# Kernel tuning notes

Measured on AMD Instinct MI355X. Metric: run time of the kernel, lower is better.

Reference implementation:

```python
import jax, jax.numpy as jnp
import numpy as np

B, S, H = 2, 2048, 1024
NH, NKV, HD = 16, 16, 64
R, KF = 16, 4
THETA = 1000000.0


def setup_inputs() -> dict:
    key = jax.random.key(0)
    ks = jax.random.split(key, 16)
    sc = 0.02
    signs = jax.random.randint(ks[13], (1, 1, 1, KF, HD // 2), 0, 2).astype(jnp.float32) * 2 - 1
    cdma = jnp.concatenate([signs, signs], axis=-1)  # [1,1,1,KF,HD]
    return {
        "hidden_states": jax.random.normal(ks[0], (B, S, H), jnp.float32),
        "position_ids": jnp.broadcast_to(jnp.arange(S, dtype=jnp.int32), (B, S)),
        "q_w": jax.random.normal(ks[1], (H, H), jnp.float32) * sc,
        "q_b": jax.random.normal(ks[2], (H,), jnp.float32) * sc,
        "k_w": jax.random.normal(ks[3], (H, H), jnp.float32) * sc,
        "k_b": jax.random.normal(ks[4], (H,), jnp.float32) * sc,
        "v_w": jax.random.normal(ks[5], (H, H), jnp.float32) * sc,
        "v_b": jax.random.normal(ks[6], (H,), jnp.float32) * sc,
        "o_w": jax.random.normal(ks[7], (H, H), jnp.float32) * sc,
        "lora_qA": jax.random.normal(ks[8], (R, H), jnp.float32) * sc,
        "lora_qB": jax.random.normal(ks[9], (H, R), jnp.float32) * sc,
        "lora_vA": jax.random.normal(ks[10], (R, H), jnp.float32) * sc,
        "lora_vB": jax.random.normal(ks[11], (H, R), jnp.float32) * sc,
        "cdma_keys": cdma,
    }


def _rope(q, k, position_ids):
    # cos/sin per HF rotary embedding, theta=1e6 (Qwen1.5)
    inv_freq = 1.0 / (THETA ** (jnp.arange(0, HD, 2, dtype=jnp.float32) / HD))  # [HD/2]
    freqs = position_ids.astype(jnp.float32)[..., None] * inv_freq  # [B,S,HD/2]
    emb = jnp.concatenate([freqs, freqs], axis=-1)  # [B,S,HD]
    cos = jnp.cos(emb)[:, None]  # [B,1,S,HD]
    sin = jnp.sin(emb)[:, None]

    def rot_half(x):
        return jnp.concatenate([-x[..., HD // 2:], x[..., :HD // 2]], axis=-1)

    return q * cos + rot_half(q) * sin, k * cos + rot_half(k) * sin


def reference(hidden_states, position_ids, q_w, q_b, k_w, k_b, v_w, v_b, o_w,
              lora_qA, lora_qB, lora_vA, lora_vB, cdma_keys):
    bsz, q_len, _ = hidden_states.shape
    # base projections + LoRA adjustments (k has no LoRA)
    q = hidden_states @ q_w.T + q_b + (hidden_states @ lora_qA.T) @ lora_qB.T
    k = hidden_states @ k_w.T + k_b
    v = hidden_states @ v_w.T + v_b + (hidden_states @ lora_vA.T) @ lora_vB.T

    q = q.reshape(bsz, q_len, NH, HD).transpose(0, 2, 1, 3)   # [B,NH,S,HD]
    k = k.reshape(bsz, q_len, NKV, HD).transpose(0, 2, 1, 3)  # [B,NKV,S,HD]
    v = v.reshape(bsz, q_len, NKV, HD).transpose(0, 2, 1, 3)

    q, k = _rope(q, k, position_ids)

    # holographic block sign-bind/sum transform (q_len divisible by KF -> no pad)
    n_slots = q_len // KF
    k_blocks = k.reshape(bsz, NKV, n_slots, KF, HD)
    v_blocks = v.reshape(bsz, NKV, n_slots, KF, HD)
    S_K = jnp.sum(k_blocks * cdma_keys, axis=3, keepdims=True)  # [B,NKV,slots,1,HD]
    S_V = jnp.sum(v_blocks * cdma_keys, axis=3, keepdims=True)
    K_noisy = (S_K * cdma_keys).reshape(bsz, NKV, q_len, HD)
    V_noisy = (S_V * cdma_keys).reshape(bsz, NKV, q_len, HD)

    scale = 1.0 / (np.sqrt(HD) * np.sqrt(KF))
    scores = jnp.einsum('bhqd,bhkd->bhqk', q, K_noisy) * scale
    causal = jnp.tril(jnp.ones((q_len, q_len), dtype=bool))
    scores = jnp.where(causal, scores, jnp.float32(-1e9))
    attn = jax.nn.softmax(scores, axis=-1)
    out = jnp.einsum('bhqk,bhkd->bhqd', attn, V_noisy)
    out = out.transpose(0, 2, 1, 3).reshape(bsz, q_len, NH * HD)
    return out @ o_w.T
```

## Files before the change

### kernel.cpp

```cpp
#include <hip/hip_runtime.h>
#include <hip/hip_bf16.h>
#include <math.h>


typedef __bf16 bf16;
typedef __attribute__((ext_vector_type(8))) __bf16 bf16x8;
typedef __attribute__((ext_vector_type(4))) float f32x4;
typedef __attribute__((ext_vector_type(2))) unsigned u32x2;

#define NB 2
#define SEQ 2048
#define HID 1024
#define NHD 16
#define HDD 64

__device__ __forceinline__ void gld_lds16(const void* g, void* l) {
  __builtin_amdgcn_global_load_lds(
      (const __attribute__((address_space(1))) void*)g,
      (__attribute__((address_space(3))) void*)l, 16, 0, 0);
}

__device__ __forceinline__ unsigned pack2bf(float a, float b) {
  unsigned short ua = __builtin_bit_cast(unsigned short, (bf16)a);
  unsigned short ub = __builtin_bit_cast(unsigned short, (bf16)b);
  return ((unsigned)ub << 16) | ua;
}

#define RB_W    12288
#define RB_HS   (RB_W + 16384)
#define RB_OW   (RB_HS + 4096)
#define RB_BIAS (RB_OW + 12)
#define RB_TAB  (RB_BIAS + 256)

__global__ __launch_bounds__(256) void prep_all(
    const float* __restrict__ hs, const float* __restrict__ ow,
    const float* __restrict__ qw, const float* __restrict__ qb,
    const float* __restrict__ kw, const float* __restrict__ kb,
    const float* __restrict__ vw, const float* __restrict__ vb,
    const float* __restrict__ qA, const float* __restrict__ qB,
    const float* __restrict__ vA, const float* __restrict__ vB,
    bf16* __restrict__ hsb, bf16* __restrict__ owb, bf16* __restrict__ Wqkv,
    float* __restrict__ bqkv, float* __restrict__ ct, float* __restrict__ st) {
  const int bid = blockIdx.x, tid = threadIdx.x;
  if (bid < RB_W) {
    int idx = bid * 256 + tid;
    int n = idx >> 10, k = idx & 1023;
    float v;
    if (n < 1024) {
      v = qw[n * 1024 + k];
#pragma unroll
      for (int r = 0; r < 16; ++r) v += qB[n * 16 + r] * qA[r * 1024 + k];
    } else if (n < 2048) {
      v = kw[(n - 1024) * 1024 + k];
    } else {
      int nn = n - 2048;
      v = vw[nn * 1024 + k];
#pragma unroll
      for (int r = 0; r < 16; ++r) v += vB[nn * 16 + r] * vA[r * 1024 + k];
    }
    int seg = k >> 6, cl = k & 63;
    int ch = (cl >> 3) ^ (n & 7);
    Wqkv[(size_t)n * 1024 + (seg << 6) + (ch << 3) + (cl & 7)] = (bf16)v;
  } else if (bid < RB_HS) {
    int idx = (bid - RB_W) * 256 + tid;
    int r = idx >> 10, c = idx & 1023;
    int seg = c >> 6, cl = c & 63;
    int ch = (cl >> 3) ^ (r & 7);
    hsb[(size_t)r * 1024 + (seg << 6) + (ch << 3) + (cl & 7)] = (bf16)hs[idx];
  } else if (bid < RB_OW) {
    int idx = (bid - RB_HS) * 256 + tid;
    int r = idx >> 10, c = idx & 1023;
    int seg = c >> 6, cl = c & 63;
    int ch = (cl >> 3) ^ (r & 7);
    owb[(size_t)r * 1024 + (seg << 6) + (ch << 3) + (cl & 7)] = (bf16)ow[idx];
  } else if (bid < RB_BIAS) {
    int i = (bid - RB_OW) * 256 + tid;
    if (i < 3072)
      bqkv[i] = (i < 1024) ? qb[i] : (i < 2048 ? kb[i - 1024] : vb[i - 2048]);
  } else {
    int idx = (bid - RB_BIAS) * 256 + tid;
    int s = idx >> 5, i = idx & 31;
    double inv = pow(1.0e6, -(double)i / 32.0);
    double a = (double)s * inv;
    ct[idx] = (float)cos(a);
    st[idx] = (float)sin(a);
  }
}

__global__ __launch_bounds__(256) void gemm_bt(
    const bf16* __restrict__ A, const bf16* __restrict__ Bw,
    const float* __restrict__ bias, bf16* __restrict__ Cb,
    float* __restrict__ Cf, int M, int N, int K) {
  __shared__ __align__(16) bf16 As[128 * 64];
  __shared__ __align__(16) bf16 Bs[128 * 64];
  const int tid = threadIdx.x;
  const int lane = tid & 63, w = tid >> 6;
  const int wm = w >> 1, wn = w & 1;
  const int l15 = lane & 15, l4 = lane >> 4;
  const int m0 = blockIdx.y * 128, n0 = blockIdx.x * 128;
  const size_t rowb = (size_t)K * 2;
  const char* gA = (const char*)A + (size_t)m0 * rowb;
  const char* gB = (const char*)Bw + (size_t)n0 * rowb;
  f32x4 acc[4][4] = {};

  for (int k0 = 0; k0 < K; k0 += 64) {
    const char* gAk = gA + k0 * 2;
    const char* gBk = gB + k0 * 2;
#pragma unroll
    for (int i = 0; i < 4; ++i) {
      int idx = i * 256 + tid;
      int row = idx >> 3, ch = idx & 7;
      gld_lds16(gAk + (size_t)row * rowb + ch * 16,
                (char*)As + (i * 256 + (w << 6)) * 16);
      gld_lds16(gBk + (size_t)row * rowb + ch * 16,
                (char*)Bs + (i * 256 + (w << 6)) * 16);
    }
    __syncthreads();
#pragma unroll
    for (int c = 0; c < 2; ++c) {
      bf16x8 af[4], bfr[4];
#pragma unroll
      for (int mi = 0; mi < 4; ++mi) {
        int row = wm * 64 + mi * 16 + l15;
        int ch = (c * 4 + l4) ^ (row & 7);
        af[mi] = *(const bf16x8*)(As + row * 64 + ch * 8);
      }
#pragma unroll
      for (int ni = 0; ni < 4; ++ni) {
        int row = wn * 64 + ni * 16 + l15;
        int ch = (c * 4 + l4) ^ (row & 7);
        bfr[ni] = *(const bf16x8*)(Bs + row * 64 + ch * 8);
      }
#pragma unroll
      for (int mi = 0; mi < 4; ++mi)
#pragma unroll
        for (int ni = 0; ni < 4; ++ni)
          acc[mi][ni] = __builtin_amdgcn_mfma_f32_16x16x32_bf16(
              af[mi], bfr[ni], acc[mi][ni], 0, 0, 0);
    }
    __syncthreads();
  }
#pragma unroll
  for (int mi = 0; mi < 4; ++mi) {
    int rbase = m0 + wm * 64 + mi * 16 + l4 * 4;
#pragma unroll
    for (int ni = 0; ni < 4; ++ni) {
      int col = n0 + wn * 64 + ni * 16 + l15;
      float badd = bias ? bias[col] : 0.0f;
#pragma unroll
      for (int r = 0; r < 4; ++r) {
        float v = acc[mi][ni][r] + badd;
        if (Cf) Cf[(size_t)(rbase + r) * N + col] = v;
        else    Cb[(size_t)(rbase + r) * N + col] = (bf16)v;
      }
    }
  }
}

__global__ __launch_bounds__(256) void rope_q(
    const bf16* __restrict__ qkv, const int* __restrict__ pos,
    const float* __restrict__ ct, const float* __restrict__ st,
    bf16* __restrict__ Qr) {
  const float SCQ = 0.0901684403f;
  int idx = blockIdx.x * 256 + threadIdx.x;
  if (idx >= NB * NHD * SEQ * 4) return;
  int ih = idx & 3, s = (idx >> 2) & 2047, h = (idx >> 13) & 15, b = idx >> 17;
  int p = pos[b * SEQ + s];
  size_t base = ((size_t)(b * SEQ + s)) * 3072 + h * 64 + ih * 8;
  bf16x8 xv = *(const bf16x8*)(qkv + base);
  bf16x8 yv = *(const bf16x8*)(qkv + base + 32);
  const float* ctp = ct + p * 32 + ih * 8;
  const float* stp = st + p * 32 + ih * 8;
  bf16x8 o0, o1;
#pragma unroll
  for (int e = 0; e < 8; ++e) {
    float x = (float)xv[e], y = (float)yv[e];
    float co = ctp[e], sn = stp[e];
    o0[e] = (bf16)((x * co - y * sn) * SCQ);
    o1[e] = (bf16)((y * co + x * sn) * SCQ);
  }
  size_t ob = ((size_t)((b * 16 + h) * SEQ + s)) * 64 + ih * 8;
  *(bf16x8*)(Qr + ob) = o0;
  *(bf16x8*)(Qr + ob + 32) = o1;
}

__global__ __launch_bounds__(256) void holo_kv(
    const bf16* __restrict__ qkv, const int* __restrict__ pos,
    const float* __restrict__ ct, const float* __restrict__ st,
    const float* __restrict__ cdma, bf16* __restrict__ Kn,
    bf16* __restrict__ Vt) {
  int idx = blockIdx.x * 256 + threadIdx.x;
  if (idx >= NB * NHD * (SEQ / 4) * 4) return;
  int ih = idx & 3, slot = (idx >> 2) & 511, h = (idx >> 11) & 15, b = idx >> 15;
  float SK[8] = {}, SK2[8] = {}, SV[8] = {}, SV2[8] = {};
#pragma unroll
  for (int f = 0; f < 4; ++f) {
    int s = slot * 4 + f;
    size_t base = ((size_t)(b * SEQ + s)) * 3072 + h * 64 + ih * 8;
    bf16x8 klo = *(const bf16x8*)(qkv + base + 1024);
    bf16x8 khi = *(const bf16x8*)(qkv + base + 1024 + 32);
    bf16x8 vlo = *(const bf16x8*)(qkv + base + 2048);
    bf16x8 vhi = *(const bf16x8*)(qkv + base + 2048 + 32);
    int p = pos[b * SEQ + s];
    const float* ctp = ct + p * 32 + ih * 8;
    const float* stp = st + p * 32 + ih * 8;
    const float* cdp = cdma + f * 64 + ih * 8;
#pragma unroll
    for (int e = 0; e < 8; ++e) {
      float cf = cdp[e];
      float kx = (float)klo[e], ky = (float)khi[e];
      float co = ctp[e], sn = stp[e];
      SK[e]  += (kx * co - ky * sn) * cf;
      SK2[e] += (ky * co + kx * sn) * cf;
      SV[e]  += (float)vlo[e] * cf;
      SV2[e] += (float)vhi[e] * cf;
    }
  }
  size_t hb = (size_t)(b * 16 + h);
#pragma unroll
  for (int f = 0; f < 4; ++f) {
    int s = slot * 4 + f;
    const float* cdp = cdma + f * 64 + ih * 8;
    bf16x8 k0, k1;
#pragma unroll
    for (int e = 0; e < 8; ++e) {
      k0[e] = (bf16)(SK[e] * cdp[e]);
      k1[e] = (bf16)(SK2[e] * cdp[e]);
    }
    size_t krow = (hb * SEQ + s) * 64;
    int ch0 = ih ^ (s & 7);
    int ch1 = (4 + ih) ^ (s & 7);
    *(bf16x8*)(Kn + krow + ch0 * 8) = k0;
    *(bf16x8*)(Kn + krow + ch1 * 8) = k1;
    int seg = s >> 6, cl = s & 63;
    size_t vcol = (size_t)(seg << 6) + (cl & 7);
#pragma unroll
    for (int e = 0; e < 8; ++e) {
      int i = ih * 8 + e;
      int vch = (cl >> 3) ^ (i & 7);
      Vt[(hb * 64 + i) * (size_t)SEQ + vcol + vch * 8] = (bf16)(SV[e] * cdp[e]);
      Vt[(hb * 64 + i + 32) * (size_t)SEQ + vcol + vch * 8] = (bf16)(SV2[e] * cdp[e]);
    }
  }
}

__global__ __launch_bounds__(256) void attn_fwd(
    const bf16* __restrict__ Qr, const bf16* __restrict__ Kn,
    const bf16* __restrict__ Vt, bf16* __restrict__ AO) {
  __shared__ __align__(16) bf16 Kt[2][128 * 64];
  __shared__ __align__(16) bf16 Vl[2][64 * 128];
  __shared__ __align__(16) bf16 Pt[4][16 * 128];
  const int pq = blockIdx.x, h = blockIdx.y, b = blockIdx.z;
  const int tid = threadIdx.x, lane = tid & 63, w = tid >> 6;
  const int l15 = lane & 15, l4 = lane >> 4;
  const size_t hd = ((size_t)(b * 16 + h)) * SEQ * 64;
  const char* gK0 = (const char*)(Kn + hd);
  const char* gV0 = (const char*)(Vt + hd);
  char* pw = (char*)&Pt[w][0];

#pragma unroll 1
  for (int phase = 0; phase < 2; ++phase) {
    const int qt = phase ? (31 - pq) : pq;
    const int q0 = qt * 64;
    const int qg = q0 + w * 16 + l15;
    const int nt = (qt >> 1) + 1;

    const bf16* qb = Qr + hd + (size_t)qg * 64;
    bf16x8 qf0 = *(const bf16x8*)(qb + l4 * 8);
    bf16x8 qf1 = *(const bf16x8*)(qb + 32 + l4 * 8);

    f32x4 oacc[4] = {};
    float m = -1e30f, lsum = 0.0f;

#pragma unroll
    for (int i = 0; i < 4; ++i)
      gld_lds16(gK0 + (i * 256 + tid) * 16,
                (char*)Kt[0] + (i * 256 + (w << 6)) * 16);
#pragma unroll
    for (int i = 0; i < 4; ++i) {
      int idx = i * 256 + tid;
      int row = idx >> 4, ch = idx & 15;
      gld_lds16(gV0 + (size_t)row * (SEQ * 2) + ch * 16,
                (char*)Vl[0] + (i * 256 + (w << 6)) * 16);
    }

#pragma unroll 1
    for (int t = 0; t < nt; ++t) {
      const int cur = t & 1;
      if (t + 1 < nt) {
        const int tn = t + 1, sb = cur ^ 1;
#pragma unroll
        for (int i = 0; i < 4; ++i)
          gld_lds16(gK0 + (size_t)tn * 16384 + (i * 256 + tid) * 16,
                    (char*)Kt[sb] + (i * 256 + (w << 6)) * 16);
#pragma unroll
        for (int i = 0; i < 4; ++i) {
          int idx = i * 256 + tid;
          int row = idx >> 4, ch = idx & 15;
          gld_lds16(gV0 + (size_t)row * (SEQ * 2) + tn * 256 + ch * 16,
                    (char*)Vl[sb] + (i * 256 + (w << 6)) * 16);
        }
        asm volatile("s_waitcnt vmcnt(8)\ns_barrier" ::: "memory");
      } else {
        asm volatile("s_waitcnt vmcnt(0)\ns_barrier" ::: "memory");
      }

      const bf16* Ktc = Kt[cur];
      const bf16* Vlc = Vl[cur];
      const int kv0 = t * 128;
      const bool lastt = (t == nt - 1);

      f32x4 sacc[8] = {};
#pragma unroll
      for (int c = 0; c < 2; ++c) {
        bf16x8 qf = c ? qf1 : qf0;
#pragma unroll
        for (int nf = 0; nf < 8; ++nf) {
          int row = nf * 16 + l15;
          int ch = (c * 4 + l4) ^ (row & 7);
          bf16x8 kf = *(const bf16x8*)(Ktc + row * 64 + ch * 8);
          sacc[nf] = __builtin_amdgcn_mfma_f32_16x16x32_bf16(kf, qf, sacc[nf], 0, 0, 0);
        }
      }

      float px[4] = {-1e30f, -1e30f, -1e30f, -1e30f};
      if (lastt) {
#pragma unroll
        for (int nf = 0; nf < 8; ++nf)
#pragma unroll
          for (int r = 0; r < 4; ++r) {
            int kvg = kv0 + nf * 16 + l4 * 4 + r;
            float v = (kvg > qg) ? -1e30f : sacc[nf][r];
            sacc[nf][r] = v;
            px[nf & 3] = fmaxf(px[nf & 3], v);
          }
      } else {
#pragma unroll
        for (int nf = 0; nf < 8; ++nf)
#pragma unroll
          for (int r = 0; r < 4; ++r) px[nf & 3] = fmaxf(px[nf & 3], sacc[nf][r]);
      }
      float pmax = fmaxf(fmaxf(px[0], px[1]), fmaxf(px[2], px[3]));
      pmax = fmaxf(pmax, __shfl_xor(pmax, 16));
      pmax = fmaxf(pmax, __shfl_xor(pmax, 32));

      if (!__all(pmax <= m)) {
        float mn = fmaxf(m, pmax);
        float al = exp2f(m - mn);
        m = mn;
        lsum *= al;
#pragma unroll
        for (int df = 0; df < 4; ++df) oacc[df] *= al;
      }
      float rs4[4] = {0.f, 0.f, 0.f, 0.f};
#pragma unroll
      for (int nf = 0; nf < 8; ++nf)
#pragma unroll
        for (int r = 0; r < 4; ++r) {
          float e = exp2f(sacc[nf][r] - m);
          sacc[nf][r] = e;
          rs4[nf & 3] += e;
        }
      float rs = (rs4[0] + rs4[1]) + (rs4[2] + rs4[3]);
      rs += __shfl_xor(rs, 16);
      rs += __shfl_xor(rs, 32);
      lsum += rs;

#pragma unroll
      for (int nf = 0; nf < 8; ++nf) {
        u32x2 u;
        u.x = pack2bf(sacc[nf][0], sacc[nf][1]);
        u.y = pack2bf(sacc[nf][2], sacc[nf][3]);
        int boff = (l15 * 256 + nf * 32 + l4 * 8) ^ ((l15 & 7) << 4);
        *(u32x2*)(pw + boff) = u;
      }

#pragma unroll
      for (int c2 = 0; c2 < 4; ++c2) {
        int pb = (l15 * 256 + c2 * 64 + l4 * 16) ^ ((l15 & 7) << 4);
        bf16x8 pf = *(const bf16x8*)(pw + pb);
        int vbyte = (c2 * 64 + l4 * 16) ^ ((l15 & 7) << 4);
#pragma unroll
        for (int df = 0; df < 4; ++df) {
          int vrow = df * 16 + l15;
          bf16x8 vf = *(const bf16x8*)((const char*)Vlc + vrow * 256 + vbyte);
          oacc[df] = __builtin_amdgcn_mfma_f32_16x16x32_bf16(vf, pf, oacc[df], 0, 0, 0);
        }
      }
      asm volatile("s_barrier" ::: "memory");
    }

    const float li = 1.0f / lsum;
    const size_t arow = ((size_t)(b * SEQ + qg)) * HID + h * 64;
    const int qk7 = qg & 7;
#pragma unroll
    for (int df = 0; df < 4; ++df)
#pragma unroll
      for (int r = 0; r < 4; ++r) {
        int d = df * 16 + l4 * 4 + r;
        int ch = (d >> 3) ^ qk7;
        AO[arow + ch * 8 + (d & 7)] = (bf16)(oacc[df][r] * li);
      }
  }
}

extern "C" void kernel_launch(void* const* d_in, const int* in_sizes, int n_in,
                              void* d_out, int out_size, void* d_ws, size_t ws_size,
                              hipStream_t stream) {
  const float* hs  = (const float*)d_in[0];
  const int* pos   = (const int*)d_in[1];
  const float* qw  = (const float*)d_in[2];
  const float* qb_ = (const float*)d_in[3];
  const float* kw  = (const float*)d_in[4];
  const float* kb_ = (const float*)d_in[5];
  const float* vw  = (const float*)d_in[6];
  const float* vb_ = (const float*)d_in[7];
  const float* ow  = (const float*)d_in[8];
  const float* qA  = (const float*)d_in[9];
  const float* qB  = (const float*)d_in[10];
  const float* vA  = (const float*)d_in[11];
  const float* vB  = (const float*)d_in[12];
  const float* cd  = (const float*)d_in[13];

  char* p = (char*)d_ws;
  auto alloc = [&](size_t bytes) {
    char* r = p; p += (bytes + 255) & ~(size_t)255; return r;
  };
  bf16* hsb   = (bf16*)alloc((size_t)4096 * 1024 * 2);
  bf16* Wqkv  = (bf16*)alloc((size_t)3072 * 1024 * 2);
  float* bqkv = (float*)alloc(3072 * 4);
  bf16* owb   = (bf16*)alloc((size_t)1024 * 1024 * 2);
  bf16* qkvb  = (bf16*)alloc((size_t)4096 * 3072 * 2);
  float* ct   = (float*)alloc((size_t)SEQ * 32 * 4);
  float* st   = (float*)alloc((size_t)SEQ * 32 * 4);
  bf16* Qrb   = (bf16*)alloc((size_t)NB * NHD * SEQ * 64 * 2);
  bf16* Knb   = (bf16*)alloc((size_t)NB * NHD * SEQ * 64 * 2);
  bf16* Vtb   = (bf16*)alloc((size_t)NB * NHD * 64 * SEQ * 2);
  bf16* AOb   = (bf16*)alloc((size_t)4096 * 1024 * 2);

  prep_all<<<dim3(RB_TAB), 256, 0, stream>>>(
      hs, ow, qw, qb_, kw, kb_, vw, vb_, qA, qB, vA, vB,
      hsb, owb, Wqkv, bqkv, ct, st);
  gemm_bt<<<dim3(3072 / 128, 4096 / 128), 256, 0, stream>>>(
      hsb, Wqkv, bqkv, qkvb, nullptr, 4096, 3072, 1024);
  rope_q<<<dim3(NB * NHD * SEQ * 4 / 256), 256, 0, stream>>>(qkvb, pos, ct, st, Qrb);
  holo_kv<<<dim3(NB * NHD * (SEQ / 4) * 4 / 256), 256, 0, stream>>>(
      qkvb, pos, ct, st, cd, Knb, Vtb);
  attn_fwd<<<dim3(16, NHD, NB), 256, 0, stream>>>(Qrb, Knb, Vtb, AOb);
  gemm_bt<<<dim3(1024 / 128, 4096 / 128), 256, 0, stream>>>(
      AOb, owb, nullptr, nullptr, (float*)d_out, 4096, 1024, 1024);
}
```

Baseline: 158.2 us.

## Fuse RoPE and holographic K/V transform into QKV GEMM epilogue

Replaces the QKV GEMM, the separate rope_q kernel and the holo_kv kernel with one GEMM whose epilogue applies bias, RoPE, the Q scale, and the block sign-bind/sum on K and V. It writes Qr, Kn and the transposed Vt directly, so the intermediate bf16 qkv buffer is no longer written and read back and two launches go away. In exchange the epilogue does scattered scalar bf16 stores and per-element table lookups, which may be less coalesced than the old vectorised kernels.

```diff
diff --git a/kernel.cpp b/kernel.cpp
--- a/kernel.cpp
+++ b/kernel.cpp
@@ -87,9 +87,149 @@
   }
 }
 
+__global__ __launch_bounds__(256) void gemm_qkv(
+    const bf16* __restrict__ A, const bf16* __restrict__ Bw,
+    const float* __restrict__ bias, const int* __restrict__ pos,
+    const float* __restrict__ ct, const float* __restrict__ st,
+    const float* __restrict__ cd, bf16* __restrict__ Qr,
+    bf16* __restrict__ Kn, bf16* __restrict__ Vt) {
+  __shared__ __align__(16) bf16 As[128 * 64];
+  __shared__ __align__(16) bf16 Bs[128 * 64];
+  const int tid = threadIdx.x;
+  const int lane = tid & 63, w = tid >> 6;
+  const int wm = w >> 1, wn = w & 1;
+  const int l15 = lane & 15, l4 = lane >> 4;
+  const int m0 = blockIdx.y * 128, n0 = blockIdx.x * 128;
+  const int K = 1024;
+  const size_t rowb = (size_t)K * 2;
+  const char* gA = (const char*)A + (size_t)m0 * rowb;
+  const char* gB = (const char*)Bw + (size_t)n0 * rowb;
+  f32x4 acc[4][4] = {};
+
+  for (int k0 = 0; k0 < K; k0 += 64) {
+    const char* gAk = gA + k0 * 2;
+    const char* gBk = gB + k0 * 2;
+#pragma unroll
+    for (int i = 0; i < 4; ++i) {
+      int idx = i * 256 + tid;
+      int row = idx >> 3, ch = idx & 7;
+      gld_lds16(gAk + (size_t)row * rowb + ch * 16,
+                (char*)As + (i * 256 + (w << 6)) * 16);
+      gld_lds16(gBk + (size_t)row * rowb + ch * 16,
+                (char*)Bs + (i * 256 + (w << 6)) * 16);
+    }
+    __syncthreads();
+#pragma unroll
+    for (int c = 0; c < 2; ++c) {
+      bf16x8 af[4], bfr[4];
+#pragma unroll
+      for (int mi = 0; mi < 4; ++mi) {
+        int row = wm * 64 + mi * 16 + l15;
+        int ch = (c * 4 + l4) ^ (row & 7);
+        af[mi] = *(const bf16x8*)(As + row * 64 + ch * 8);
+      }
+#pragma unroll
+      for (int ni = 0; ni < 4; ++ni) {
+        int row = wn * 64 + ni * 16 + l15;
+        int ch = (c * 4 + l4) ^ (row & 7);
+        bfr[ni] = *(const bf16x8*)(Bs + row * 64 + ch * 8);
+      }
+#pragma unroll
+      for (int mi = 0; mi < 4; ++mi)
+#pragma unroll
+        for (int ni = 0; ni < 4; ++ni)
+          acc[mi][ni] = __builtin_amdgcn_mfma_f32_16x16x32_bf16(
+              af[mi], bfr[ni], acc[mi][ni], 0, 0, 0);
+    }
+    __syncthreads();
+  }
+
+  const float SCQ = 0.0901684403f;
+  const int nb0 = n0 + wn * 64;
+  const int region = nb0 >> 10;
+  const int h = (nb0 & 1023) >> 6;
+
+#pragma unroll
+  for (int mi = 0; mi < 4; ++mi) {
+    const int sg0 = m0 + wm * 64 + mi * 16 + l4 * 4;
+    const int b = sg0 >> 11, s0 = sg0 & 2047;
+    const size_t hb = (size_t)(b * 16 + h);
+    if (region == 0) {
+#pragma unroll
+      for (int ni = 0; ni < 2; ++ni) {
+        const int i = ni * 16 + l15;
+        const float bx = bias[nb0 + i];
+        const float by = bias[nb0 + i + 32];
+#pragma unroll
+        for (int r = 0; r < 4; ++r) {
+          int s = s0 + r;
+          int p = pos[sg0 + r];
+          float co = ct[p * 32 + i], sn = st[p * 32 + i];
+          float x = acc[mi][ni][r] + bx;
+          float y = acc[mi][ni + 2][r] + by;
+          size_t ob = (hb * SEQ + s) * 64 + i;
+          Qr[ob]      = (bf16)((x * co - y * sn) * SCQ);
+          Qr[ob + 32] = (bf16)((y * co + x * sn) * SCQ);
+        }
+      }
+    } else if (region == 1) {
+#pragma unroll
+      for (int ni = 0; ni < 2; ++ni) {
+        const int i = ni * 16 + l15;
+        const float bx = bias[nb0 + i];
+        const float by = bias[nb0 + i + 32];
+        float cdv[4];
+        float SK = 0.f, SK2 = 0.f, rot0[4], rot1[4];
+#pragma unroll
+        for (int r = 0; r < 4; ++r) {
+          int p = pos[sg0 + r];
+          float co = ct[p * 32 + i], sn = st[p * 32 + i];
+          float x = acc[mi][ni][r] + bx;
+          float y = acc[mi][ni + 2][r] + by;
+          rot0[r] = x * co - y * sn;
+          rot1[r] = y * co + x * sn;
+          float cf = cd[r * 64 + i];
+          cdv[r] = cf;
+          SK  += rot0[r] * cf;
+          SK2 += rot1[r] * cf;
+        }
+#pragma unroll
+        for (int r = 0; r < 4; ++r) {
+          int s = s0 + r;
+          size_t krow = (hb * SEQ + s) * 64;
+          int ch0 = (i >> 3) ^ (s & 7);
+          int ch1 = (4 + (i >> 3)) ^ (s & 7);
+          Kn[krow + ch0 * 8 + (i & 7)] = (bf16)(SK * cdv[r]);
+          Kn[krow + ch1 * 8 + (i & 7)] = (bf16)(SK2 * cdv[r]);
+        }
+      }
+    } else {
+#pragma unroll
+      for (int ni = 0; ni < 4; ++ni) {
+        const int i = ni * 16 + l15;
+        const float bv = bias[nb0 + i];
+        float cdv[4];
+        float SV = 0.f;
+#pragma unroll
+        for (int r = 0; r < 4; ++r) {
+          float cf = cd[r * 64 + i];
+          cdv[r] = cf;
+          SV += (acc[mi][ni][r] + bv) * cf;
+        }
+        int seg = s0 >> 6, cl = s0 & 63;
+        int vch = (cl >> 3) ^ (i & 7);
+        size_t voff = (hb * 64 + i) * (size_t)SEQ + (seg << 6) + vch * 8 + (cl & 7);
+        u32x2 u;
+        u.x = pack2bf(SV * cdv[0], SV * cdv[1]);
+        u.y = pack2bf(SV * cdv[2], SV * cdv[3]);
+        *(u32x2*)(Vt + voff) = u;
+      }
+    }
+  }
+}
+
 __global__ __launch_bounds__(256) void gemm_bt(
     const bf16* __restrict__ A, const bf16* __restrict__ Bw,
-    const float* __restrict__ bias, bf16* __restrict__ Cb,
     float* __restrict__ Cf, int M, int N, int K) {
   __shared__ __align__(16) bf16 As[128 * 64];
   __shared__ __align__(16) bf16 Bs[128 * 64];
@@ -146,100 +286,9 @@
 #pragma unroll
     for (int ni = 0; ni < 4; ++ni) {
       int col = n0 + wn * 64 + ni * 16 + l15;
-      float badd = bias ? bias[col] : 0.0f;
-#pragma unroll
-      for (int r = 0; r < 4; ++r) {
-        float v = acc[mi][ni][r] + badd;
-        if (Cf) Cf[(size_t)(rbase + r) * N + col] = v;
-        else    Cb[(size_t)(rbase + r) * N + col] = (bf16)v;
-      }
-    }
-  }
-}
-
-__global__ __launch_bounds__(256) void rope_q(
-    const bf16* __restrict__ qkv, const int* __restrict__ pos,
-    const float* __restrict__ ct, const float* __restrict__ st,
-    bf16* __restrict__ Qr) {
-  const float SCQ = 0.0901684403f;
-  int idx = blockIdx.x * 256 + threadIdx.x;
-  if (idx >= NB * NHD * SEQ * 4) return;
-  int ih = idx & 3, s = (idx >> 2) & 2047, h = (idx >> 13) & 15, b = idx >> 17;
-  int p = pos[b * SEQ + s];
-  size_t base = ((size_t)(b * SEQ + s)) * 3072 + h * 64 + ih * 8;
-  bf16x8 xv = *(const bf16x8*)(qkv + base);
-  bf16x8 yv = *(const bf16x8*)(qkv + base + 32);
-  const float* ctp = ct + p * 32 + ih * 8;
-  const float* stp = st + p * 32 + ih * 8;
-  bf16x8 o0, o1;
-#pragma unroll
-  for (int e = 0; e < 8; ++e) {
-    float x = (float)xv[e], y = (float)yv[e];
-    float co = ctp[e], sn = stp[e];
-    o0[e] = (bf16)((x * co - y * sn) * SCQ);
-    o1[e] = (bf16)((y * co + x * sn) * SCQ);
-  }
-  size_t ob = ((size_t)((b * 16 + h) * SEQ + s)) * 64 + ih * 8;
-  *(bf16x8*)(Qr + ob) = o0;
-  *(bf16x8*)(Qr + ob + 32) = o1;
-}
-
-__global__ __launch_bounds__(256) void holo_kv(
-    const bf16* __restrict__ qkv, const int* __restrict__ pos,
-    const float* __restrict__ ct, const float* __restrict__ st,
-    const float* __restrict__ cdma, bf16* __restrict__ Kn,
-    bf16* __restrict__ Vt) {
-  int idx = blockIdx.x * 256 + threadIdx.x;
-  if (idx >= NB * NHD * (SEQ / 4) * 4) return;
-  int ih = idx & 3, slot = (idx >> 2) & 511, h = (idx >> 11) & 15, b = idx >> 15;
-  float SK[8] = {}, SK2[8] = {}, SV[8] = {}, SV2[8] = {};
-#pragma unroll
-  for (int f = 0; f < 4; ++f) {
-    int s = slot * 4 + f;
-    size_t base = ((size_t)(b * SEQ + s)) * 3072 + h * 64 + ih * 8;
-    bf16x8 klo = *(const bf16x8*)(qkv + base + 1024);
-    bf16x8 khi = *(const bf16x8*)(qkv + base + 1024 + 32);
-    bf16x8 vlo = *(const bf16x8*)(qkv + base + 2048);
-    bf16x8 vhi = *(const bf16x8*)(qkv + base + 2048 + 32);
-    int p = pos[b * SEQ + s];
-    const float* ctp = ct + p * 32 + ih * 8;
-    const float* stp = st + p * 32 + ih * 8;
-    const float* cdp = cdma + f * 64 + ih * 8;
-#pragma unroll
-    for (int e = 0; e < 8; ++e) {
-      float cf = cdp[e];
-      float kx = (float)klo[e], ky = (float)khi[e];
-      float co = ctp[e], sn = stp[e];
-      SK[e]  += (kx * co - ky * sn) * cf;
-      SK2[e] += (ky * co + kx * sn) * cf;
-      SV[e]  += (float)vlo[e] * cf;
-      SV2[e] += (float)vhi[e] * cf;
-    }
-  }
-  size_t hb = (size_t)(b * 16 + h);
-#pragma unroll
-  for (int f = 0; f < 4; ++f) {
-    int s = slot * 4 + f;
-    const float* cdp = cdma + f * 64 + ih * 8;
-    bf16x8 k0, k1;
-#pragma unroll
-    for (int e = 0; e < 8; ++e) {
-      k0[e] = (bf16)(SK[e] * cdp[e]);
-      k1[e] = (bf16)(SK2[e] * cdp[e]);
-    }
-    size_t krow = (hb * SEQ + s) * 64;
-    int ch0 = ih ^ (s & 7);
-    int ch1 = (4 + ih) ^ (s & 7);
-    *(bf16x8*)(Kn + krow + ch0 * 8) = k0;
-    *(bf16x8*)(Kn + krow + ch1 * 8) = k1;
-    int seg = s >> 6, cl = s & 63;
-    size_t vcol = (size_t)(seg << 6) + (cl & 7);
-#pragma unroll
-    for (int e = 0; e < 8; ++e) {
-      int i = ih * 8 + e;
-      int vch = (cl >> 3) ^ (i & 7);
-      Vt[(hb * 64 + i) * (size_t)SEQ + vcol + vch * 8] = (bf16)(SV[e] * cdp[e]);
-      Vt[(hb * 64 + i + 32) * (size_t)SEQ + vcol + vch * 8] = (bf16)(SV2[e] * cdp[e]);
+#pragma unroll
+      for (int r = 0; r < 4; ++r)
+        Cf[(size_t)(rbase + r) * N + col] = acc[mi][ni][r];
     }
   }
 }
@@ -430,7 +479,6 @@
   bf16* Wqkv  = (bf16*)alloc((size_t)3072 * 1024 * 2);
   float* bqkv = (float*)alloc(3072 * 4);
   bf16* owb   = (bf16*)alloc((size_t)1024 * 1024 * 2);
-  bf16* qkvb  = (bf16*)alloc((size_t)4096 * 3072 * 2);
   float* ct   = (float*)alloc((size_t)SEQ * 32 * 4);
   float* st   = (float*)alloc((size_t)SEQ * 32 * 4);
   bf16* Qrb   = (bf16*)alloc((size_t)NB * NHD * SEQ * 64 * 2);
@@ -441,12 +489,9 @@
   prep_all<<<dim3(RB_TAB), 256, 0, stream>>>(
       hs, ow, qw, qb_, kw, kb_, vw, vb_, qA, qB, vA, vB,
       hsb, owb, Wqkv, bqkv, ct, st);
-  gemm_bt<<<dim3(3072 / 128, 4096 / 128), 256, 0, stream>>>(
-      hsb, Wqkv, bqkv, qkvb, nullptr, 4096, 3072, 1024);
-  rope_q<<<dim3(NB * NHD * SEQ * 4 / 256), 256, 0, stream>>>(qkvb, pos, ct, st, Qrb);
-  holo_kv<<<dim3(NB * NHD * (SEQ / 4) * 4 / 256), 256, 0, stream>>>(
-      qkvb, pos, ct, st, cd, Knb, Vtb);
+  gemm_qkv<<<dim3(3072 / 128, 4096 / 128), 256, 0, stream>>>(
+      hsb, Wqkv, bqkv, pos, ct, st, cd, Qrb, Knb, Vtb);
   attn_fwd<<<dim3(16, NHD, NB), 256, 0, stream>>>(Qrb, Knb, Vtb, AOb);
   gemm_bt<<<dim3(1024 / 128, 4096 / 128), 256, 0, stream>>>(
-      AOb, owb, nullptr, nullptr, (float*)d_out, 4096, 1024, 1024);
-}
+      AOb, owb, (float*)d_out, 4096, 1024, 1024);
+}
```

New measurement: 169.4 us. 1.07x slower.
